# Optimization experiments

Hardware: AMD Instinct MI355X
Metric: run time of the kernel (lower is better)

Reference implementation:

```python
import jax, jax.numpy as jnp
import numpy as np
import math

B, S, NUM_HEADS, HEAD_SIZE = 4, 2048, 16, 64
EMB = NUM_HEADS * HEAD_SIZE  # 1024


def setup_inputs() -> dict:
    key = jax.random.key(0)
    k0, k1, k2, k3 = jax.random.split(key, 4)
    scale = 1.0 / math.sqrt(EMB)
    return {
        "hidden_states": jax.random.normal(k0, (B, S, EMB), dtype=jnp.float32),
        "qkv_w": jax.random.normal(k1, (EMB, 3 * EMB), dtype=jnp.float32) * scale,
        "qkv_b": jnp.zeros((3 * EMB,), dtype=jnp.float32),
        "wo_w": jax.random.normal(k2, (EMB, EMB), dtype=jnp.float32) * scale,
        "wo_b": jnp.zeros((EMB,), dtype=jnp.float32),
        "mask": jax.random.randint(k3, (B, S), 0, 2, dtype=jnp.int64)
        if jax.config.jax_enable_x64 else jax.random.randint(k3, (B, S), 0, 2, dtype=jnp.int32),
    }


def reference(hidden_states, qkv_w, qkv_b, wo_w, wo_b, mask):
    b, s, e = hidden_states.shape
    h, d = NUM_HEADS, HEAD_SIZE
    qkv = hidden_states @ qkv_w + qkv_b            # [b, s, 3e]
    q, k, v = jnp.split(qkv, 3, axis=-1)
    # split heads: [b, s, e] -> [b, h, s, d]
    split = lambda t: t.reshape(b, s, h, d).transpose(0, 2, 1, 3)
    q, k, v = split(q), split(k), split(v)
    # naive attention: full [b, h, s, s] score matrix, scaled by sqrt(head_size)
    scores = jnp.einsum("bhqd,bhkd->bhqk", q, k) / jnp.sqrt(jnp.asarray(d, q.dtype))
    # torch code repeats the [b, s] padding mask into [b, h, s, s]; it masks KEYS:
    # position j with mask[b, j] == 0 is -inf for all queries and heads.
    scores = jnp.where(mask[:, None, None, :] == 0, -jnp.inf, scores)
    attn = jax.nn.softmax(scores, axis=-1)
    out = jnp.einsum("bhqk,bhkd->bhqd", attn, v)   # [b, h, s, d]
    out = out.transpose(0, 2, 1, 3).reshape(b, s, e)  # merge heads
    return out @ wo_w + wo_b
```

## Files before the change

### kernel.cpp

```cpp
#include <hip/hip_runtime.h>
#include <math.h>

typedef __bf16 bf16;
typedef __bf16 bf16x4 __attribute__((ext_vector_type(4)));
typedef __bf16 bf16x8 __attribute__((ext_vector_type(8)));
typedef _Float16 f16;
typedef _Float16 f16x8 __attribute__((ext_vector_type(8)));
typedef float floatx4 __attribute__((ext_vector_type(4)));

#define MFMA_BF16(a, b, c) __builtin_amdgcn_mfma_f32_16x16x32_bf16((a), (b), (c), 0, 0, 0)
#define MFMA_F16(a, b, c) __builtin_amdgcn_mfma_f32_16x16x32_f16((a), (b), (c), 0, 0, 0)

__device__ inline void gload16(const void* g, void* l) {
  __builtin_amdgcn_global_load_lds(
      (const __attribute__((address_space(1))) void*)g,
      (__attribute__((address_space(3))) void*)l, 16, 0, 0);
}

__device__ inline int detect_i64(const void* m_) {
  const unsigned int* m = (const unsigned int*)m_;
  unsigned int o = 0;
  for (int i = 1; i < 256; i += 2) o |= m[i];
  return o == 0;
}

__device__ inline int xcd_swizzle(int bid, int nwg) {
  return (bid & 7) * (nwg >> 3) + (bid >> 3);
}

__global__ void wsplit(const float* __restrict__ in, f16* __restrict__ out,
                       int R, int C) {
  __shared__ float tile[32][33];
  int bx = blockIdx.x * 32, by = blockIdx.y * 32;
  int tx = threadIdx.x, ty = threadIdx.y;
#pragma unroll
  for (int i = 0; i < 32; i += 8)
    tile[ty + i][tx] = in[(size_t)(by + ty + i) * C + bx + tx];
  __syncthreads();
#pragma unroll
  for (int i = 0; i < 32; i += 8) {
    float x = tile[tx][ty + i];
    size_t oi = (size_t)(bx + ty + i) * R + by + tx;
    out[oi] = (f16)x;
  }
}

template <int MODE>
__global__ __launch_bounds__(256) void gemm(
    const void* __restrict__ Av, const f16* __restrict__ Bg,
    const float* __restrict__ bias, void* __restrict__ Cq,
    bf16* __restrict__ Ck, bf16* __restrict__ Cv, int M, int N, int K) {
  constexpr int APAD = (MODE == 1) ? 40 : 32;
  __shared__ __align__(16) f16 Ah[2][128][APAD];
  __shared__ __align__(16) f16 Bs[2][128][32];

  int tid = threadIdx.x;
  int wave = tid >> 6, lane = tid & 63;
  int quad = lane >> 4, c = lane & 15;
  int wrow = (wave >> 1) * 64, wcol = (wave & 1) * 64;

  int nwg = gridDim.x * gridDim.y;
  int bid = blockIdx.x + gridDim.x * blockIdx.y;
  int nb = xcd_swizzle(bid, nwg);
  int m0 = (nb / gridDim.x) * 128, n0 = (nb % gridDim.x) * 128;

  int srow = lane >> 2;
  int ql8 = (((lane & 3) ^ ((lane >> 3) & 3)) * 8);
  int rswz = (c >> 1) & 3;

  floatx4 zero4 = {0.f, 0.f, 0.f, 0.f};
  floatx4 acc[4][4];
#pragma unroll
  for (int i = 0; i < 4; ++i)
#pragma unroll
    for (int j = 0; j < 4; ++j) acc[i][j] = zero4;

  floatx4 aR[4];

#define STAGE_B(buf, kk)                                                    \
  {                                                                         \
    _Pragma("unroll") for (int u = 0; u < 2; ++u) {                         \
      int ch = wave * 2 + u;                                                \
      size_t gi = (size_t)(n0 + ch * 16 + srow) * K + (kk) + ql8;           \
      gload16(&Bg[gi], &Bs[buf][ch * 16][0]);                               \
    }                                                                       \
  }
#define STAGE_A_DMA(buf, kk)                                                \
  {                                                                         \
    _Pragma("unroll") for (int u = 0; u < 2; ++u) {                         \
      int ch = wave * 2 + u;                                                \
      size_t gi = (size_t)(m0 + ch * 16 + srow) * K + (kk) + ql8;           \
      gload16((const f16*)Av + gi, &Ah[buf][ch * 16][0]);                   \
    }                                                                       \
  }
#define ISSUE_A(kk)                                                         \
  {                                                                         \
    const float* Af = (const float*)Av;                                     \
    _Pragma("unroll") for (int p = 0; p < 2; ++p) {                         \
      int off = p * 2048 + tid * 8;                                         \
      int r = off >> 5, cc = off & 31;                                      \
      size_t gi = (size_t)(m0 + r) * K + (kk) + cc;                         \
      aR[p * 2] = *(const floatx4*)&Af[gi];                                 \
      aR[p * 2 + 1] = *(const floatx4*)&Af[gi + 4];                         \
    }                                                                       \
  }
#define WRITE_A(buf)                                                        \
  {                                                                         \
    _Pragma("unroll") for (int p = 0; p < 2; ++p) {                         \
      int off = p * 2048 + tid * 8;                                         \
      int r = off >> 5, cc = off & 31;                                      \
      f16x8 h;                                                              \
      _Pragma("unroll") for (int uu = 0; uu < 4; ++uu) {                    \
        h[uu] = (f16)aR[p * 2][uu];                                         \
        h[4 + uu] = (f16)aR[p * 2 + 1][uu];                                 \
      }                                                                     \
      *(f16x8*)&Ah[buf][r][cc] = h;                                         \
    }                                                                       \
  }

  STAGE_B(0, 0);
  if constexpr (MODE == 1) {
    ISSUE_A(0);
    WRITE_A(0);
  } else {
    STAGE_A_DMA(0, 0);
  }
  __syncthreads();

  int nk = K / 32;
  int cur = 0;
  for (int t = 0; t < nk; ++t) {
    int kn = (t + 1) * 32;
    bool has_next = (t + 1 < nk);
    if (has_next) {
      STAGE_B(cur ^ 1, kn);
      if constexpr (MODE == 1) {
        ISSUE_A(kn);
      } else {
        STAGE_A_DMA(cur ^ 1, kn);
      }
    }

    f16x8 ah[4], bh[4];
#pragma unroll
    for (int i = 0; i < 4; ++i) {
      if constexpr (MODE == 1)
        ah[i] = *(const f16x8*)&Ah[cur][wrow + i * 16 + c][quad * 8];
      else
        ah[i] = *(const f16x8*)&Ah[cur][wrow + i * 16 + c][(quad ^ rswz) * 8];
    }
#pragma unroll
    for (int j = 0; j < 4; ++j)
      bh[j] = *(const f16x8*)&Bs[cur][wcol + j * 16 + c][(quad ^ rswz) * 8];
#pragma unroll
    for (int i = 0; i < 4; ++i)
#pragma unroll
      for (int j = 0; j < 4; ++j)
        acc[i][j] = MFMA_F16(ah[i], bh[j], acc[i][j]);

    if (has_next) {
      if constexpr (MODE == 1) WRITE_A(cur ^ 1);
      __syncthreads();
      cur ^= 1;
    }
  }
#undef STAGE_B
#undef STAGE_A_DMA
#undef ISSUE_A
#undef WRITE_A

#pragma unroll
  for (int i = 0; i < 4; ++i) {
#pragma unroll
    for (int j = 0; j < 4; ++j) {
      int col = n0 + wcol + j * 16 + c;
      float bvv = bias[col];
#pragma unroll
      for (int r = 0; r < 4; ++r) {
        int row = m0 + wrow + i * 16 + quad * 4 + r;
        float v = acc[i][j][r] + bvv;
        if constexpr (MODE == 0) {
          ((float*)Cq)[(size_t)row * N + col] = v;
        } else {
          int which = col >> 10;
          int h = (col >> 6) & 15;
          int d = col & 63;
          int b = row >> 11;
          int s = row & 2047;
          if (which == 0) {
            ((bf16*)Cq)[((size_t)(b * 2048 + s)) * 1024 + h * 64 + d] = (bf16)v;
          } else if (which == 1) {
            Ck[((size_t)(b * 16 + h) * 2048 + s) * 64 + d] = (bf16)v;
          } else {
            Cv[((size_t)(b * 16 + h) * 64 + d) * 2048 + s] = (bf16)v;
          }
        }
      }
    }
  }
}

__global__ __launch_bounds__(256) void attn_fused(
    bf16* QO, const bf16* __restrict__ Kg, const bf16* __restrict__ Vg,
    const void* __restrict__ mask) {
  __shared__ __align__(16) bf16 Ks[64][72];
  __shared__ __align__(16) bf16 Vts[64][72];
  __shared__ __align__(16) bf16 Ps[64][72];
  __shared__ __align__(16) float abuf[64];

  const int i64 = detect_i64(mask);

  int tid = threadIdx.x;
  int wave = tid >> 6, lane = tid & 63;
  int quad = lane >> 4, c = lane & 15;

  int nwg = gridDim.x * gridDim.y;
  int bid = blockIdx.x + gridDim.x * blockIdx.y;
  int nb = xcd_swizzle(bid, nwg);
  int qt = nb & 31, bh = nb >> 5;

  int b = bh >> 4, h = bh & 15;
  int q0 = qt * 64;
  bf16* Qp = QO + (size_t)b * 2048 * 1024 + h * 64;
  const bf16* Kp = Kg + (size_t)bh * 2048 * 64;
  const bf16* Vp = Vg + (size_t)bh * 64 * 2048;

  bf16x8 qf[2];
#pragma unroll
  for (int ds = 0; ds < 2; ++ds)
    qf[ds] = *(const bf16x8*)&Qp[(size_t)(q0 + wave * 16 + c) * 1024 +
                                 ds * 32 + quad * 8];

  float lacc = 0.f;
  floatx4 zero4 = {0.f, 0.f, 0.f, 0.f};
  floatx4 o[4];
#pragma unroll
  for (int jd = 0; jd < 4; ++jd) o[jd] = zero4;

#pragma unroll
  for (int p = 0; p < 2; ++p) {
    int off = p * 2048 + tid * 8;
    int r = off >> 6, cc = off & 63;
    *(bf16x8*)&Ks[r][cc] = *(const bf16x8*)&Kp[(size_t)r * 64 + cc];
  }
  if (tid < 64) {
    int idx = b * 2048 + tid;
    int mv = i64 ? (int)((const long long*)mask)[idx]
                 : ((const int*)mask)[idx];
    abuf[tid] = mv ? -12.0f : -1e30f;
  }
  __syncthreads();

  for (int kt = 0; kt < 32; ++kt) {
    int k0 = kt * 64;

    bf16x8 vstage[2];
#pragma unroll
    for (int p = 0; p < 2; ++p) {
      int off = p * 2048 + tid * 8;
      int r = off >> 6, cc = off & 63;
      vstage[p] = *(const bf16x8*)&Vp[(size_t)r * 2048 + k0 + cc];
    }

    floatx4 st[4];
#pragma unroll
    for (int j = 0; j < 4; ++j) st[j] = zero4;
#pragma unroll
    for (int ds = 0; ds < 2; ++ds) {
#pragma unroll
      for (int j = 0; j < 4; ++j) {
        bf16x8 ak = *(const bf16x8*)&Ks[j * 16 + c][ds * 32 + quad * 8];
        st[j] = MFMA_BF16(ak, qf[ds], st[j]);
      }
    }

#pragma unroll
    for (int j = 0; j < 4; ++j) {
      floatx4 am = *(const floatx4*)&abuf[j * 16 + quad * 4];
      bf16x4 pk;
#pragma unroll
      for (int r = 0; r < 4; ++r) {
        float pv = __expf(fmaf(st[j][r], 0.125f, am[r]));
        pk[r] = (bf16)pv;
        lacc += pv;
      }
      *(bf16x4*)&Ps[wave * 16 + c][j * 16 + quad * 4] = pk;
    }

#pragma unroll
    for (int p = 0; p < 2; ++p) {
      int off = p * 2048 + tid * 8;
      int r = off >> 6, cc = off & 63;
      *(bf16x8*)&Vts[r][cc] = vstage[p];
    }
    __syncthreads();

    bf16x8 kstage[2];
    bool more = (kt + 1) < 32;
    int kn = k0 + 64;
    if (more) {
#pragma unroll
      for (int p = 0; p < 2; ++p) {
        int off = p * 2048 + tid * 8;
        int r = off >> 6, cc = off & 63;
        kstage[p] = *(const bf16x8*)&Kp[(size_t)(kn + r) * 64 + cc];
      }
    }

#pragma unroll
    for (int kk = 0; kk < 64; kk += 32) {
      bf16x8 ap = *(const bf16x8*)&Ps[wave * 16 + c][kk + quad * 8];
#pragma unroll
      for (int jd = 0; jd < 4; ++jd) {
        bf16x8 bv = *(const bf16x8*)&Vts[jd * 16 + c][kk + quad * 8];
        o[jd] = MFMA_BF16(ap, bv, o[jd]);
      }
    }

    if (more) {
#pragma unroll
      for (int p = 0; p < 2; ++p) {
        int off = p * 2048 + tid * 8;
        int r = off >> 6, cc = off & 63;
        *(bf16x8*)&Ks[r][cc] = kstage[p];
      }
      if (tid < 64) {
        int idx = b * 2048 + kn + tid;
        int mv = i64 ? (int)((const long long*)mask)[idx]
                     : ((const int*)mask)[idx];
        abuf[tid] = mv ? -12.0f : -1e30f;
      }
      __syncthreads();
    }
  }

  lacc += __shfl_xor(lacc, 16, 64);
  lacc += __shfl_xor(lacc, 32, 64);

#pragma unroll
  for (int r = 0; r < 4; ++r) {
    float lr = __shfl(lacc, quad * 4 + r, 64);
    float inv_l = 1.0f / fmaxf(lr, 1e-30f);
    int row = q0 + wave * 16 + quad * 4 + r;
#pragma unroll
    for (int jd = 0; jd < 4; ++jd) {
      float ov = o[jd][r] * inv_l;
      *(f16*)&Qp[(size_t)row * 1024 + jd * 16 + c] = (f16)ov;
    }
  }
}

extern "C" void kernel_launch(void* const* d_in, const int* in_sizes, int n_in,
                              void* d_out, int out_size, void* d_ws, size_t ws_size,
                              hipStream_t stream) {
  (void)in_sizes; (void)n_in; (void)out_size;
  const float* hs    = (const float*)d_in[0];
  const float* qkv_w = (const float*)d_in[1];
  const float* qkv_b = (const float*)d_in[2];
  const float* wo_w  = (const float*)d_in[3];
  const float* wo_b  = (const float*)d_in[4];
  const void*  mask  = d_in[5];

  if (ws_size < 33554432) return;

  bf16* kbuf = (bf16*)d_ws;
  f16*  wq   = (f16*)((char*)d_ws + 16777216);
  f16*  wo   = (f16*)((char*)d_ws + 16777216 + 6291456);
  bf16* vbuf = (bf16*)d_out + (size_t)8388608;
  f16*  obuf = (f16*)d_ws;

  wsplit<<<dim3(96, 32), dim3(32, 8), 0, stream>>>(qkv_w, wq, 1024, 3072);
  wsplit<<<dim3(32, 32), dim3(32, 8), 0, stream>>>(wo_w, wo, 1024, 1024);

  gemm<1><<<dim3(24, 64), 256, 0, stream>>>(
      hs, wq, qkv_b, d_out, kbuf, vbuf, 8192, 3072, 1024);

  attn_fused<<<dim3(32, 64), 256, 0, stream>>>(
      (bf16*)d_out, kbuf, vbuf, mask);

  (void)hipMemcpyAsync(d_ws, d_out, (size_t)16777216, hipMemcpyDeviceToDevice,
                       stream);

  gemm<0><<<dim3(8, 64), 256, 0, stream>>>(
      obuf, wo, wo_b, d_out, nullptr, nullptr, 8192, 1024, 1024);
}
```

Measured before the change: 373.2 us.

## Use 32x32 MFMA with 128-query tiles and keep P in registers

After: 362.9 us. 2.8% less time.

```diff
diff --git a/kernel.cpp b/kernel.cpp
--- a/kernel.cpp
+++ b/kernel.cpp
@@ -5,11 +5,31 @@
 typedef __bf16 bf16x4 __attribute__((ext_vector_type(4)));
 typedef __bf16 bf16x8 __attribute__((ext_vector_type(8)));
 typedef _Float16 f16;
+typedef _Float16 f16x4 __attribute__((ext_vector_type(4)));
 typedef _Float16 f16x8 __attribute__((ext_vector_type(8)));
 typedef float floatx4 __attribute__((ext_vector_type(4)));
+typedef float floatx16 __attribute__((ext_vector_type(16)));
+typedef short shortx4 __attribute__((ext_vector_type(4)));
 
 #define MFMA_BF16(a, b, c) __builtin_amdgcn_mfma_f32_16x16x32_bf16((a), (b), (c), 0, 0, 0)
 #define MFMA_F16(a, b, c) __builtin_amdgcn_mfma_f32_16x16x32_f16((a), (b), (c), 0, 0, 0)
+#define MFMA32_BF16(a, b, c) __builtin_amdgcn_mfma_f32_32x32x16_bf16((a), (b), (c), 0, 0, 0)
+
+__device__ inline floatx16 MFMA_PV32(bf16x4 a, bf16x4 b, floatx16 c) {
+#if __has_builtin(__builtin_amdgcn_mfma_f32_32x32x8_bf16)
+  return __builtin_amdgcn_mfma_f32_32x32x8_bf16(a, b, c, 0, 0, 0);
+#elif __has_builtin(__builtin_amdgcn_mfma_f32_32x32x8bf16_1k)
+  shortx4 as, bs;
+  __builtin_memcpy(&as, &a, 8);
+  __builtin_memcpy(&bs, &b, 8);
+  return __builtin_amdgcn_mfma_f32_32x32x8bf16_1k(as, bs, c, 0, 0, 0);
+#else
+  bf16 z = (bf16)0.f;
+  bf16x8 a8 = {a[0], a[1], a[2], a[3], z, z, z, z};
+  bf16x8 b8 = {b[0], b[1], b[2], b[3], z, z, z, z};
+  return MFMA32_BF16(a8, b8, c);
+#endif
+}
 
 __device__ inline void gload16(const void* g, void* l) {
   __builtin_amdgcn_global_load_lds(
@@ -205,37 +225,46 @@
     const void* __restrict__ mask) {
   __shared__ __align__(16) bf16 Ks[64][72];
   __shared__ __align__(16) bf16 Vts[64][72];
-  __shared__ __align__(16) bf16 Ps[64][72];
-  __shared__ __align__(16) float abuf[64];
+  __shared__ __align__(16) float abuf_all[2048];
 
   const int i64 = detect_i64(mask);
 
   int tid = threadIdx.x;
   int wave = tid >> 6, lane = tid & 63;
-  int quad = lane >> 4, c = lane & 15;
+  int l31 = lane & 31, hi = lane >> 5;
 
   int nwg = gridDim.x * gridDim.y;
   int bid = blockIdx.x + gridDim.x * blockIdx.y;
   int nb = xcd_swizzle(bid, nwg);
-  int qt = nb & 31, bh = nb >> 5;
+  int qt = nb & 15, bh = nb >> 4;
 
   int b = bh >> 4, h = bh & 15;
-  int q0 = qt * 64;
+  int q0 = qt * 128;
   bf16* Qp = QO + (size_t)b * 2048 * 1024 + h * 64;
   const bf16* Kp = Kg + (size_t)bh * 2048 * 64;
   const bf16* Vp = Vg + (size_t)bh * 64 * 2048;
 
-  bf16x8 qf[2];
-#pragma unroll
-  for (int ds = 0; ds < 2; ++ds)
-    qf[ds] = *(const bf16x8*)&Qp[(size_t)(q0 + wave * 16 + c) * 1024 +
-                                 ds * 32 + quad * 8];
-
+#pragma unroll
+  for (int i = 0; i < 8; ++i) {
+    int key = tid * 8 + i;
+    int idx = b * 2048 + key;
+    int mv = i64 ? (int)((const long long*)mask)[idx]
+                 : ((const int*)mask)[idx];
+    abuf_all[key] = mv ? -12.0f : -1e30f;
+  }
+
+  int qrow = q0 + wave * 32 + l31;
+  bf16x8 qf[4];
+#pragma unroll
+  for (int ds = 0; ds < 4; ++ds)
+    qf[ds] = *(const bf16x8*)&Qp[(size_t)qrow * 1024 + ds * 16 + hi * 8];
+
+  floatx16 o[2];
+#pragma unroll
+  for (int dt = 0; dt < 2; ++dt)
+#pragma unroll
+    for (int i = 0; i < 16; ++i) o[dt][i] = 0.f;
   float lacc = 0.f;
-  floatx4 zero4 = {0.f, 0.f, 0.f, 0.f};
-  floatx4 o[4];
-#pragma unroll
-  for (int jd = 0; jd < 4; ++jd) o[jd] = zero4;
 
 #pragma unroll
   for (int p = 0; p < 2; ++p) {
@@ -243,13 +272,9 @@
     int r = off >> 6, cc = off & 63;
     *(bf16x8*)&Ks[r][cc] = *(const bf16x8*)&Kp[(size_t)r * 64 + cc];
   }
-  if (tid < 64) {
-    int idx = b * 2048 + tid;
-    int mv = i64 ? (int)((const long long*)mask)[idx]
-                 : ((const int*)mask)[idx];
-    abuf[tid] = mv ? -12.0f : -1e30f;
-  }
   __syncthreads();
+
+  bf16x4 pk[8];
 
   for (int kt = 0; kt < 32; ++kt) {
     int k0 = kt * 64;
@@ -262,29 +287,28 @@
       vstage[p] = *(const bf16x8*)&Vp[(size_t)r * 2048 + k0 + cc];
     }
 
-    floatx4 st[4];
-#pragma unroll
-    for (int j = 0; j < 4; ++j) st[j] = zero4;
-#pragma unroll
-    for (int ds = 0; ds < 2; ++ds) {
-#pragma unroll
-      for (int j = 0; j < 4; ++j) {
-        bf16x8 ak = *(const bf16x8*)&Ks[j * 16 + c][ds * 32 + quad * 8];
-        st[j] = MFMA_BF16(ak, qf[ds], st[j]);
-      }
-    }
-
-#pragma unroll
-    for (int j = 0; j < 4; ++j) {
-      floatx4 am = *(const floatx4*)&abuf[j * 16 + quad * 4];
-      bf16x4 pk;
-#pragma unroll
-      for (int r = 0; r < 4; ++r) {
-        float pv = __expf(fmaf(st[j][r], 0.125f, am[r]));
-        pk[r] = (bf16)pv;
-        lacc += pv;
-      }
-      *(bf16x4*)&Ps[wave * 16 + c][j * 16 + quad * 4] = pk;
+#pragma unroll
+    for (int t2 = 0; t2 < 2; ++t2) {
+      floatx16 sr;
+#pragma unroll
+      for (int i = 0; i < 16; ++i) sr[i] = 0.f;
+#pragma unroll
+      for (int ds = 0; ds < 4; ++ds) {
+        bf16x8 ak = *(const bf16x8*)&Ks[t2 * 32 + l31][ds * 16 + hi * 8];
+        sr = MFMA32_BF16(ak, qf[ds], sr);
+      }
+#pragma unroll
+      for (int s = 0; s < 4; ++s) {
+        floatx4 am = *(const floatx4*)&abuf_all[k0 + t2 * 32 + s * 8 + hi * 4];
+        bf16x4 p4;
+#pragma unroll
+        for (int j = 0; j < 4; ++j) {
+          float pv = __expf(fmaf(sr[s * 4 + j], 0.125f, am[j]));
+          lacc += pv;
+          p4[j] = (bf16)pv;
+        }
+        pk[t2 * 4 + s] = p4;
+      }
     }
 
 #pragma unroll
@@ -308,12 +332,11 @@
     }
 
 #pragma unroll
-    for (int kk = 0; kk < 64; kk += 32) {
-      bf16x8 ap = *(const bf16x8*)&Ps[wave * 16 + c][kk + quad * 8];
-#pragma unroll
-      for (int jd = 0; jd < 4; ++jd) {
-        bf16x8 bv = *(const bf16x8*)&Vts[jd * 16 + c][kk + quad * 8];
-        o[jd] = MFMA_BF16(ap, bv, o[jd]);
+    for (int ss = 0; ss < 8; ++ss) {
+#pragma unroll
+      for (int dt = 0; dt < 2; ++dt) {
+        bf16x4 av = *(const bf16x4*)&Vts[dt * 32 + l31][ss * 8 + hi * 4];
+        o[dt] = MFMA_PV32(av, pk[ss], o[dt]);
       }
     }
 
@@ -324,28 +347,22 @@
         int r = off >> 6, cc = off & 63;
         *(bf16x8*)&Ks[r][cc] = kstage[p];
       }
-      if (tid < 64) {
-        int idx = b * 2048 + kn + tid;
-        int mv = i64 ? (int)((const long long*)mask)[idx]
-                     : ((const int*)mask)[idx];
-        abuf[tid] = mv ? -12.0f : -1e30f;
-      }
       __syncthreads();
     }
   }
 
-  lacc += __shfl_xor(lacc, 16, 64);
   lacc += __shfl_xor(lacc, 32, 64);
-
-#pragma unroll
-  for (int r = 0; r < 4; ++r) {
-    float lr = __shfl(lacc, quad * 4 + r, 64);
-    float inv_l = 1.0f / fmaxf(lr, 1e-30f);
-    int row = q0 + wave * 16 + quad * 4 + r;
-#pragma unroll
-    for (int jd = 0; jd < 4; ++jd) {
-      float ov = o[jd][r] * inv_l;
-      *(f16*)&Qp[(size_t)row * 1024 + jd * 16 + c] = (f16)ov;
+  float inv = 1.0f / fmaxf(lacc, 1e-30f);
+
+#pragma unroll
+  for (int dt = 0; dt < 2; ++dt) {
+#pragma unroll
+    for (int t = 0; t < 4; ++t) {
+      f16x4 out;
+#pragma unroll
+      for (int j = 0; j < 4; ++j) out[j] = (f16)(o[dt][t * 4 + j] * inv);
+      int d0 = dt * 32 + t * 8 + hi * 4;
+      *(f16x4*)((f16*)&Qp[(size_t)qrow * 1024] + d0) = out;
     }
   }
 }
@@ -375,7 +392,7 @@
   gemm<1><<<dim3(24, 64), 256, 0, stream>>>(
       hs, wq, qkv_b, d_out, kbuf, vbuf, 8192, 3072, 1024);
 
-  attn_fused<<<dim3(32, 64), 256, 0, stream>>>(
+  attn_fused<<<dim3(16, 64), 256, 0, stream>>>(
       (bf16*)d_out, kbuf, vbuf, mask);
 
   (void)hipMemcpyAsync(d_ws, d_out, (size_t)16777216, hipMemcpyDeviceToDevice,
```
